# Performance work log

Hardware: AMD Instinct MI355X
Metric: run time of the kernel (lower is better)

Reference implementation:

```python
import jax, jax.numpy as jnp
import numpy as np

FEAT = 128
N_RBF = 20
CUTOFF = 5.0
N_GRAPHS = 128
ATOMS = 64
N_ATOMS = N_GRAPHS * ATOMS  # 8192
N_EDGES = N_ATOMS * 32      # 262144


def setup_inputs() -> dict:
    key = jax.random.key(0)
    ks = jax.random.split(key, 12)
    s_j = jax.random.normal(ks[0], (N_ATOMS, FEAT), jnp.float32)
    v_j = jax.random.normal(ks[1], (N_ATOMS, FEAT, 3), jnp.float32)
    r_ij = jax.random.normal(ks[2], (N_EDGES, 3), jnp.float32) * 1.5
    nbrs = jax.random.randint(ks[3], (N_EDGES, 2), 0, N_ATOMS, dtype=jnp.int32)
    num_atoms = jnp.full((N_GRAPHS,), ATOMS, dtype=jnp.int32)
    sc = 0.05
    W1 = jax.random.normal(ks[4], (FEAT, FEAT), jnp.float32) * sc
    b1 = jnp.zeros((FEAT,), jnp.float32)
    W2 = jax.random.normal(ks[5], (FEAT, 3 * FEAT), jnp.float32) * sc
    b2 = jnp.zeros((3 * FEAT,), jnp.float32)
    Wr = jax.random.normal(ks[6], (N_RBF, 3 * FEAT), jnp.float32) * sc
    br = jnp.zeros((3 * FEAT,), jnp.float32)
    Wd = jax.random.normal(ks[7], (FEAT, 3 * FEAT), jnp.float32) * sc
    bd = jnp.zeros((3 * FEAT,), jnp.float32)
    return {"s_j": s_j, "v_j": v_j, "r_ij": r_ij, "nbrs": nbrs,
            "num_atoms": num_atoms, "W1": W1, "b1": b1, "W2": W2, "b2": b2,
            "Wr": Wr, "br": br, "Wd": Wd, "bd": bd}


def _forward(s_j, v_j, r_ij, nbrs, W1, b1, W2, b2, Wr, br, Wd, bd):
    # preprocess_r
    dist = jnp.linalg.norm(r_ij, axis=-1)            # [E]
    unit = r_ij / dist[:, None]                      # [E,3]

    # InvariantMessage: per-atom MLP, gather at nbrs[:,1], times radial filter
    phi = jax.nn.silu(s_j @ W1 + b1) @ W2 + b2       # [N, 3F]
    phi_e = phi[nbrs[:, 1]]                          # [E, 3F]
    n = jnp.arange(1, N_RBF + 1, dtype=jnp.float32)
    rbf = jnp.sin(n[None, :] * jnp.pi * dist[:, None] / CUTOFF) / dist[:, None]  # [E, n_rbf]
    env = jnp.where(dist < CUTOFF, 0.5 * (jnp.cos(jnp.pi * dist / CUTOFF) + 1.0), 0.0)
    w_s = (rbf @ Wr + br) * env[:, None]             # [E, 3F]
    inv_out = (phi_e * w_s).reshape(-1, 3, FEAT)     # [E, 3, F]

    split_0 = inv_out[:, 0, :][..., None]            # [E, F, 1]
    split_1 = inv_out[:, 1, :]                       # [E, F]
    split_2 = inv_out[:, 2, :][..., None]            # [E, F, 1]

    unit_add = split_2 * unit[:, None, :]            # [E, F, 3]
    delta_v_ij = unit_add + split_0 * v_j[nbrs[:, 1]]  # [E, F, 3]
    delta_s_ij = split_1                             # [E, F]

    seg = nbrs[:, 0]
    delta_v_i = jax.ops.segment_sum(delta_v_ij, seg, num_segments=N_ATOMS)
    delta_s_l = jax.ops.segment_sum(delta_s_ij, seg, num_segments=N_ATOMS)

    # NonLocalInteraction: per-graph exact softmax attention (uniform graph size)
    qkv = s_j @ Wd + bd                              # [N, 3F]
    Q, K, V = jnp.split(qkv, 3, axis=-1)
    Qb = Q.reshape(N_GRAPHS, ATOMS, FEAT)
    Kb = K.reshape(N_GRAPHS, ATOMS, FEAT)
    Vb = V.reshape(N_GRAPHS, ATOMS, FEAT)
    scores = jnp.einsum('bqf,bkf->bqk', Qb, Kb) / jnp.sqrt(jnp.float32(FEAT))
    att = jnp.einsum('bqk,bkf->bqf', jax.nn.softmax(scores, axis=-1), Vb)
    delta_s_nl = att.reshape(N_ATOMS, FEAT)

    delta_s_i = delta_s_l + delta_s_nl
    return delta_s_i, delta_v_i


def reference(s_j, v_j, r_ij, nbrs, num_atoms, W1, b1, W2, b2, Wr, br, Wd, bd):
    # num_atoms is uniform (ATOMS per graph); attention is batched accordingly.
    return _forward(s_j, v_j, r_ij, nbrs, W1, b1, W2, b2, Wr, br, Wd, bd)
```

## Files before the change

kernel.cpp:

```cpp
#include <hip/hip_runtime.h>
#include <hip/hip_bf16.h>
#include <cstdint>

#define FEAT    128
#define NRBF    20
#define NATOMS  8192
#define NEDGES  262144
#define NGRAPH  128
#define APG     64
#define PI_F    3.14159265358979323846f
#define CUTOFF_F 5.0f
#define QTUS    ((size_t)NATOMS * 32 * 6)
#define APW     4

typedef unsigned int uint_t;
typedef unsigned short ushort_t;
typedef __attribute__((ext_vector_type(4))) float f32x4;
typedef __attribute__((ext_vector_type(4))) short short4v;
typedef __attribute__((ext_vector_type(8))) short short8;
struct U3 { uint_t x, y, z; };

__device__ __forceinline__ float bflo(uint_t u) { return __uint_as_float(u << 16); }
__device__ __forceinline__ float bfhi(uint_t u) { return __uint_as_float(u & 0xffff0000u); }
__device__ __forceinline__ float bfus(ushort_t u) { return __uint_as_float((uint_t)u << 16); }
__device__ __forceinline__ ushort_t f2bf(float f) {
  uint_t u = __float_as_uint(f);
  return (ushort_t)((u + 0x7fffu + ((u >> 16) & 1u)) >> 16);
}
__device__ __forceinline__ uint_t pack2(float lo, float hi) {
  return (uint_t)f2bf(lo) | ((uint_t)f2bf(hi) << 16);
}

__device__ __forceinline__ ushort_t swz_elem(const float* __restrict__ W, int N,
                                             int NT, int i) {
  int jj = i & 7, lane = (i >> 3) & 63, tile = i >> 9;
  int ks = tile / NT, ctg = tile - ks * NT;
  int g = lane >> 4, q = lane & 15;
  int k = 32 * ks + 4 * g + (jj & 3) + 16 * (jj >> 2);
  int c = 16 * ctg + q;
  return f2bf(W[(size_t)k * N + c]);
}

__global__ void prep_kernel(const float* __restrict__ v_j, const float* __restrict__ W1,
                            const float* __restrict__ W2, const float* __restrict__ Wd,
                            const float* __restrict__ Wr, const float* __restrict__ br,
                            const int* __restrict__ nbrs,
                            ushort_t* __restrict__ PV, ushort_t* __restrict__ w1s,
                            ushort_t* __restrict__ w2s, ushort_t* __restrict__ wds,
                            ushort_t* __restrict__ wrs, int* __restrict__ counts) {
  int i = blockIdx.x * 256 + threadIdx.x;
  if (i < NATOMS * FEAT) {
    int j = i >> 7, f = i & 127;
    int tbl = f >> 5, fl = f & 31;
    const float* vp = v_j + (size_t)i * 3;
    uint_t* o = reinterpret_cast<uint_t*>(PV + (size_t)tbl * QTUS + ((size_t)j * 32 + fl) * 6);
    o[0] = 0u;
    o[1] = pack2(0.f, vp[0]);
    o[2] = pack2(vp[1], vp[2]);
    return;
  }
  i -= NATOMS * FEAT;
  if (i < 16384) { w1s[i] = swz_elem(W1, 128, 8, i); return; }
  i -= 16384;
  if (i < 49152) { w2s[i] = swz_elem(W2, 384, 24, i); return; }
  i -= 49152;
  if (i < 49152) { wds[i] = swz_elem(Wd, 384, 24, i); return; }
  i -= 49152;
  if (i < 12288) {
    int jj = i & 7, lane = (i >> 3) & 63, ct = i >> 9;
    int g = lane >> 4, q = lane & 15;
    int k = 4 * g + (jj & 3) + 16 * (jj >> 2);
    int f = 16 * ct + q;
    float v = (k < NRBF) ? Wr[k * 384 + f] : (k == NRBF ? br[f] : 0.f);
    wrs[i] = f2bf(v);
    return;
  }
  i -= 12288;
  if (i < NEDGES) atomicAdd(&counts[nbrs[2 * i]], 1);
}

__global__ __launch_bounds__(256) void gemm_big(
    const float* __restrict__ s_j, const ushort_t* __restrict__ w1s,
    const float* __restrict__ b1, const ushort_t* __restrict__ w2s,
    const float* __restrict__ b2, const ushort_t* __restrict__ wds,
    const float* __restrict__ bd, ushort_t* __restrict__ PV,
    float* __restrict__ Qf, ushort_t* __restrict__ kvbf) {
  __shared__ ushort_t Buf[64][136];
  const int t = threadIdx.x;
  const int r0 = blockIdx.x * 64;
  const int y = blockIdx.y;
  const int w = t >> 6, l = t & 63, g = l >> 4, q = l & 15;

  for (int i = t; i < 64 * 32; i += 256) {
    int r = i >> 5, k4 = i & 31;
    float4 v = *reinterpret_cast<const float4*>(s_j + (size_t)(r0 + r) * 128 + 4 * k4);
    ushort4 o = {f2bf(v.x), f2bf(v.y), f2bf(v.z), f2bf(v.w)};
    *reinterpret_cast<ushort4*>(&Buf[r][4 * k4]) = o;
  }
  __syncthreads();

  short8 afr[4];
  #pragma unroll
  for (int ks = 0; ks < 4; ++ks) {
    const ushort_t* ap = &Buf[16 * w + q][32 * ks + 4 * g];
    short4v alo = *reinterpret_cast<const short4v*>(ap);
    short4v ahi = *reinterpret_cast<const short4v*>(ap + 16);
    afr[ks] = short8{alo[0], alo[1], alo[2], alo[3], ahi[0], ahi[1], ahi[2], ahi[3]};
  }

  if (y >= 6) {
    const int yy = y - 6;
    #pragma unroll
    for (int ct = 0; ct < 4; ++ct) {
      f32x4 acc = {};
      #pragma unroll
      for (int ks = 0; ks < 4; ++ks) {
        short8 bf = *reinterpret_cast<const short8*>(
            wds + ((size_t)(ks * 24 + yy * 4 + ct) * 64 + l) * 8);
        acc = __builtin_amdgcn_mfma_f32_16x16x32_bf16(afr[ks], bf, acc, 0, 0, 0);
      }
      int col = yy * 64 + 16 * ct + q;
      float bb = bd[col];
      #pragma unroll
      for (int r = 0; r < 4; ++r) {
        float o = acc[r] + bb;
        int row = r0 + 16 * w + 4 * g + r;
        if (col < 128) Qf[(size_t)row * 128 + col] = o;
        else           kvbf[(size_t)row * 256 + col - 128] = f2bf(o);
      }
    }
    return;
  }

  __syncthreads();
  #pragma unroll
  for (int ct = 0; ct < 8; ++ct) {
    f32x4 acc = {};
    #pragma unroll
    for (int ks = 0; ks < 4; ++ks) {
      short8 bf = *reinterpret_cast<const short8*>(
          w1s + ((size_t)(ks * 8 + ct) * 64 + l) * 8);
      acc = __builtin_amdgcn_mfma_f32_16x16x32_bf16(afr[ks], bf, acc, 0, 0, 0);
    }
    float bb = b1[16 * ct + q];
    #pragma unroll
    for (int r = 0; r < 4; ++r) {
      float o = acc[r] + bb;
      o = o / (1.f + __expf(-o));
      Buf[16 * w + 4 * g + r][16 * ct + q] = f2bf(o);
    }
  }
  __syncthreads();

  short8 hfr[4];
  #pragma unroll
  for (int ks = 0; ks < 4; ++ks) {
    const ushort_t* ap = &Buf[16 * w + q][32 * ks + 4 * g];
    short4v alo = *reinterpret_cast<const short4v*>(ap);
    short4v ahi = *reinterpret_cast<const short4v*>(ap + 16);
    hfr[ks] = short8{alo[0], alo[1], alo[2], alo[3], ahi[0], ahi[1], ahi[2], ahi[3]};
  }
  #pragma unroll
  for (int ct = 0; ct < 4; ++ct) {
    f32x4 acc = {};
    #pragma unroll
    for (int ks = 0; ks < 4; ++ks) {
      short8 bf = *reinterpret_cast<const short8*>(
          w2s + ((size_t)(ks * 24 + y * 4 + ct) * 64 + l) * 8);
      acc = __builtin_amdgcn_mfma_f32_16x16x32_bf16(hfr[ks], bf, acc, 0, 0, 0);
    }
    int col = y * 64 + 16 * ct + q;
    float bb = b2[col];
    int f = col & 127, s = col >> 7;
    int tbl = f >> 5, fl = f & 31;
    #pragma unroll
    for (int r = 0; r < 4; ++r) {
      float o = acc[r] + bb;
      int row = r0 + 16 * w + 4 * g + r;
      PV[(size_t)tbl * QTUS + ((size_t)row * 32 + fl) * 6 + s] = f2bf(o);
    }
  }
}

__global__ __launch_bounds__(1024) void scan_kernel(
    const int* __restrict__ counts, int* __restrict__ offs, int* __restrict__ cursor) {
  __shared__ int part[1024];
  const int t = threadIdx.x;
  int local[8];
  int s = 0;
  #pragma unroll
  for (int i = 0; i < 8; ++i) { local[i] = counts[t * 8 + i]; s += local[i]; }
  part[t] = s;
  __syncthreads();
  for (int off = 1; off < 1024; off <<= 1) {
    int v = part[t];
    int add = (t >= off) ? part[t - off] : 0;
    __syncthreads();
    part[t] = v + add;
    __syncthreads();
  }
  int excl = part[t] - s;
  #pragma unroll
  for (int i = 0; i < 8; ++i) {
    offs[t * 8 + i] = excl;
    cursor[t * 8 + i] = excl;
    excl += local[i];
  }
  if (t == 1023) offs[NATOMS] = excl;
}

__global__ void scatter_kernel(const int* __restrict__ nbrs, const float* __restrict__ r_ij,
                               int* __restrict__ cursor, uint4* __restrict__ erec) {
  int e = blockIdx.x * blockDim.x + threadIdx.x;
  if (e < NEDGES) {
    int2 nb = *reinterpret_cast<const int2*>(nbrs + 2 * e);
    int pos = atomicAdd(&cursor[nb.x], 1);
    const float* rp = r_ij + 3 * e;
    erec[pos] = make_uint4((uint_t)nb.y, __float_as_uint(rp[0]),
                           __float_as_uint(rp[1]), __float_as_uint(rp[2]));
  }
}

__global__ __launch_bounds__(256) void edge_mfma8(
    const uint4* __restrict__ erec, const int* __restrict__ offs,
    const ushort_t* __restrict__ PV, const ushort_t* __restrict__ wrs,
    float* __restrict__ out_s, float* __restrict__ out_v) {
  __shared__ short8 sW[6 * 64];
  const int t = threadIdx.x;
  const int qtr = blockIdx.x & 3;
  for (int i = t; i < 6 * 64; i += 256) {
    int tl = i >> 6, l2 = i & 63;
    int s = tl >> 1, c = tl & 1;
    sW[i] = *reinterpret_cast<const short8*>(
        wrs + ((size_t)(s * 8 + 2 * qtr + c) * 64 + l2) * 8);
  }
  __syncthreads();

  const int w = t >> 6, l = t & 63, g = l >> 4, q = l & 15;
  const int a0 = ((blockIdx.x >> 2) * 4 + w) * APW;
  const float c1 = PI_F / CUTOFF_F;
  const char* PVb = reinterpret_cast<const char*>(PV) + (size_t)qtr * QTUS * 2;

  int eb = offs[a0];
  int end = offs[a0 + 1];
  uint4 er = make_uint4(0u, 0u, 0u, 0u);
  if (eb + q < end) er = erec[eb + q];

  for (int aidx = 0; aidx < APW; ++aidx) {
    const int end_next = (aidx + 1 < APW) ? offs[a0 + aidx + 2] : 0;
    float ds0 = 0.f, ds1 = 0.f;
    float dv[2][3] = {};

    for (;;) {
      const bool last = (eb + 16 >= end);
      const int neb = last ? end : (eb + 16);
      const int nend = last ? ((aidx + 1 < APW) ? end_next : neb) : end;
      uint4 ern = make_uint4(0u, 0u, 0u, 0u);
      if (neb + q < nend) ern = erec[neb + q];

      float ang = 0.f, ie = 0.f, env = 0.f, u0 = 0.f, u1 = 0.f, u2 = 0.f;
      int jn = 0;
      if (eb + q < end) {
        jn = (int)er.x;
        float x = __uint_as_float(er.y), y = __uint_as_float(er.z), z = __uint_as_float(er.w);
        float d = sqrtf(x * x + y * y + z * z);
        float inv = 1.f / d;
        ang = c1 * d;
        env = (d < CUTOFF_F) ? 0.5f * (__cosf(ang) + 1.f) : 0.f;
        ie = inv * env;
        u0 = x * inv; u1 = y * inv; u2 = z * inv;
      }
      const char* pb[4];
      float ub[4][3];
      #pragma unroll
      for (int r = 0; r < 4; ++r) {
        int src = 4 * g + r;
        int jr = __shfl(jn, src, 64);
        ub[r][0] = __shfl(u0, src, 64);
        ub[r][1] = __shfl(u1, src, 64);
        ub[r][2] = __shfl(u2, src, 64);
        pb[r] = PVb + (size_t)jr * 384 + (size_t)q * 12;
      }
      U3 ld[2][4];
      #pragma unroll
      for (int c = 0; c < 2; ++c)
        #pragma unroll
        for (int r = 0; r < 4; ++r)
          ld[c][r] = *reinterpret_cast<const U3*>(pb[r] + (size_t)c * 192);
      short8 af;
      #pragma unroll
      for (int jj = 0; jj < 8; ++jj) {
        int k = 4 * g + (jj & 3) + 16 * (jj >> 2);
        float v = (k < NRBF) ? ie * __sinf((float)(k + 1) * ang)
                             : (k == NRBF ? env : 0.f);
        af[jj] = (short)f2bf(v);
      }
      #pragma unroll
      for (int c = 0; c < 2; ++c) {
        short8 b0 = sW[(0 * 2 + c) * 64 + l];
        short8 b1 = sW[(1 * 2 + c) * 64 + l];
        short8 b2 = sW[(2 * 2 + c) * 64 + l];
        f32x4 z4 = {0.f, 0.f, 0.f, 0.f};
        f32x4 cs0 = __builtin_amdgcn_mfma_f32_16x16x32_bf16(af, b0, z4, 0, 0, 0);
        f32x4 cs1 = __builtin_amdgcn_mfma_f32_16x16x32_bf16(af, b1, z4, 0, 0, 0);
        f32x4 cs2 = __builtin_amdgcn_mfma_f32_16x16x32_bf16(af, b2, z4, 0, 0, 0);
        #pragma unroll
        for (int r = 0; r < 4; ++r) {
          U3 u = ld[c][r];
          float p0 = bflo(u.x), p1 = bfhi(u.x);
          float p2 = bflo(u.y), v0 = bfhi(u.y);
          float v1 = bflo(u.z), v2 = bfhi(u.z);
          float pw0 = p0 * cs0[r];
          if (c == 0) ds0 += p1 * cs1[r]; else ds1 += p1 * cs1[r];
          float pw2 = p2 * cs2[r];
          dv[c][0] += pw0 * v0 + pw2 * ub[r][0];
          dv[c][1] += pw0 * v1 + pw2 * ub[r][1];
          dv[c][2] += pw0 * v2 + pw2 * ub[r][2];
        }
      }
      er = ern;
      eb = neb;
      if (last) break;
    }

    float r0v = ds0, r1v = ds1;
    r0v += __shfl_xor(r0v, 16, 64); r0v += __shfl_xor(r0v, 32, 64);
    r1v += __shfl_xor(r1v, 16, 64); r1v += __shfl_xor(r1v, 32, 64);
    float dvr[2][3];
    #pragma unroll
    for (int c = 0; c < 2; ++c)
      #pragma unroll
      for (int cc = 0; cc < 3; ++cc) {
        float y = dv[c][cc];
        y += __shfl_xor(y, 16, 64); y += __shfl_xor(y, 32, 64);
        dvr[c][cc] = y;
      }
    if (g < 2) {
      int atom = a0 + aidx;
      float sv = (g == 0) ? r0v : r1v;
      float d0 = (g == 0) ? dvr[0][0] : dvr[1][0];
      float d1 = (g == 0) ? dvr[0][1] : dvr[1][1];
      float d2 = (g == 0) ? dvr[0][2] : dvr[1][2];
      int f = 32 * qtr + 16 * g + q;
      out_s[(size_t)atom * FEAT + f] = sv;
      float* ov = out_v + (size_t)atom * 384 + (size_t)f * 3;
      ov[0] = d0; ov[1] = d1; ov[2] = d2;
    }
    end = end_next;
  }
}

__device__ __forceinline__ float wave_max64(float v) {
  #pragma unroll
  for (int m = 32; m > 0; m >>= 1) v = fmaxf(v, __shfl_xor(v, m, 64));
  return v;
}
__device__ __forceinline__ float wave_sum64(float v) {
  #pragma unroll
  for (int m = 32; m > 0; m >>= 1) v += __shfl_xor(v, m, 64);
  return v;
}

__global__ __launch_bounds__(256) void attn_kernel(const float* __restrict__ Qf,
                                                   const ushort_t* __restrict__ kvbf,
                                                   float* __restrict__ out_s) {
  __shared__ float4 Ks4[64 * 32];
  __shared__ float  Vs[64][130];
  __shared__ float  Ps[4][4][64];
  const int b = blockIdx.x >> 2, quad = blockIdx.x & 3;
  const int t = threadIdx.x;
  const float* qbase = Qf + (size_t)b * APG * 128;
  const ushort_t* kvb = kvbf + (size_t)b * APG * 256;

  for (int i = t; i < 64 * 32; i += 256) {
    int a = i >> 5, gg = i & 31;
    ushort4 k4 = *reinterpret_cast<const ushort4*>(kvb + a * 256 + 4 * gg);
    float4 kf = {bfus(k4.x), bfus(k4.y), bfus(k4.z), bfus(k4.w)};
    Ks4[a * 32 + (gg ^ (a & 7))] = kf;
  }
  for (int i = t; i < 64 * 32; i += 256) {
    int a = i >> 5, gg = i & 31;
    ushort4 v4 = *reinterpret_cast<const ushort4*>(kvb + a * 256 + 128 + 4 * gg);
    Vs[a][4 * gg + 0] = bfus(v4.x); Vs[a][4 * gg + 1] = bfus(v4.y);
    Vs[a][4 * gg + 2] = bfus(v4.z); Vs[a][4 * gg + 3] = bfus(v4.w);
  }
  __syncthreads();

  const int w = t >> 6, l = t & 63;
  const int qq = 4 * quad + w;
  const float scale = 0.08838834764831845f;

  const float* q0p = qbase + (size_t)(4 * qq + 0) * 128;
  const float* q1p = qbase + (size_t)(4 * qq + 1) * 128;
  const float* q2p = qbase + (size_t)(4 * qq + 2) * 128;
  const float* q3p = qbase + (size_t)(4 * qq + 3) * 128;
  float s0 = 0.f, s1 = 0.f, s2 = 0.f, s3 = 0.f;
  #pragma unroll 8
  for (int i = 0; i < 32; ++i) {
    float4 k = Ks4[l * 32 + (i ^ (l & 7))];
    float4 q0 = *reinterpret_cast<const float4*>(q0p + 4 * i);
    float4 q1 = *reinterpret_cast<const float4*>(q1p + 4 * i);
    float4 q2 = *reinterpret_cast<const float4*>(q2p + 4 * i);
    float4 q3 = *reinterpret_cast<const float4*>(q3p + 4 * i);
    s0 += q0.x * k.x + q0.y * k.y + q0.z * k.z + q0.w * k.w;
    s1 += q1.x * k.x + q1.y * k.y + q1.z * k.z + q1.w * k.w;
    s2 += q2.x * k.x + q2.y * k.y + q2.z * k.z + q2.w * k.w;
    s3 += q3.x * k.x + q3.y * k.y + q3.z * k.z + q3.w * k.w;
  }
  s0 *= scale; s1 *= scale; s2 *= scale; s3 *= scale;

  float p0 = __expf(s0 - wave_max64(s0));
  float p1 = __expf(s1 - wave_max64(s1));
  float p2 = __expf(s2 - wave_max64(s2));
  float p3 = __expf(s3 - wave_max64(s3));
  p0 /= wave_sum64(p0); p1 /= wave_sum64(p1);
  p2 /= wave_sum64(p2); p3 /= wave_sum64(p3);

  Ps[w][0][l] = p0; Ps[w][1][l] = p1; Ps[w][2][l] = p2; Ps[w][3][l] = p3;
  __threadfence_block();

  float a00 = 0.f, a01 = 0.f, a10 = 0.f, a11 = 0.f;
  float a20 = 0.f, a21 = 0.f, a30 = 0.f, a31 = 0.f;
  for (int a = 0; a < 64; ++a) {
    float2 v = *reinterpret_cast<const float2*>(&Vs[a][2 * l]);
    float pa0 = Ps[w][0][a], pa1 = Ps[w][1][a];
    float pa2 = Ps[w][2][a], pa3 = Ps[w][3][a];
    a00 += pa0 * v.x; a01 += pa0 * v.y;
    a10 += pa1 * v.x; a11 += pa1 * v.y;
    a20 += pa2 * v.x; a21 += pa2 * v.y;
    a30 += pa3 * v.x; a31 += pa3 * v.y;
  }
  size_t row0 = (size_t)(b * APG + 4 * qq) * FEAT + 2 * l;
  float2* o0 = reinterpret_cast<float2*>(out_s + row0);
  float2* o1 = reinterpret_cast<float2*>(out_s + row0 + FEAT);
  float2* o2 = reinterpret_cast<float2*>(out_s + row0 + 2 * FEAT);
  float2* o3 = reinterpret_cast<float2*>(out_s + row0 + 3 * FEAT);
  float2 c0 = *o0; c0.x += a00; c0.y += a01; *o0 = c0;
  float2 c1 = *o1; c1.x += a10; c1.y += a11; *o1 = c1;
  float2 c2 = *o2; c2.x += a20; c2.y += a21; *o2 = c2;
  float2 c3 = *o3; c3.x += a30; c3.y += a31; *o3 = c3;
}

extern "C" void kernel_launch(void* const* d_in, const int* in_sizes, int n_in,
                              void* d_out, int out_size, void* d_ws, size_t ws_size,
                              hipStream_t stream) {
  const float* s_j  = (const float*)d_in[0];
  const float* v_j  = (const float*)d_in[1];
  const float* r_ij = (const float*)d_in[2];
  const int*   nbrs = (const int*)d_in[3];
  const float* W1   = (const float*)d_in[5];
  const float* b1   = (const float*)d_in[6];
  const float* W2   = (const float*)d_in[7];
  const float* b2   = (const float*)d_in[8];
  const float* Wr   = (const float*)d_in[9];
  const float* br   = (const float*)d_in[10];
  const float* Wd   = (const float*)d_in[11];
  const float* bd   = (const float*)d_in[12];

  float* out_s = (float*)d_out;
  float* out_v = out_s + (size_t)NATOMS * FEAT;

  float*    Qf   = (float*)d_ws;
  ushort_t* kvbf = (ushort_t*)(Qf + NATOMS * FEAT);
  ushort_t* PV   = kvbf + (size_t)NATOMS * 256;
  ushort_t* w1s  = PV + 4 * QTUS;
  ushort_t* w2s  = w1s + 16384;
  ushort_t* wds  = w2s + 49152;
  ushort_t* wrs  = wds + 49152;
  uint4*    erec = (uint4*)(wrs + 12288);
  int* offs   = (int*)(erec + NEDGES);
  int* cursor = offs + (NATOMS + 1);
  int* counts = cursor + NATOMS;

  hipMemsetAsync(counts, 0, NATOMS * sizeof(int), stream);

  int prep_total = NATOMS * FEAT + 16384 + 49152 + 49152 + 12288 + NEDGES;
  prep_kernel<<<(prep_total + 255) / 256, 256, 0, stream>>>(
      v_j, W1, W2, Wd, Wr, br, nbrs, PV, w1s, w2s, wds, wrs, counts);

  scan_kernel<<<1, 1024, 0, stream>>>(counts, offs, cursor);
  scatter_kernel<<<NEDGES / 256, 256, 0, stream>>>(nbrs, r_ij, cursor, erec);

  gemm_big<<<dim3(NATOMS / 64, 12), 256, 0, stream>>>(
      s_j, w1s, b1, w2s, b2, wds, bd, PV, Qf, kvbf);

  edge_mfma8<<<NATOMS / APW, 256, 0, stream>>>(erec, offs, PV, wrs, out_s, out_v);
  attn_kernel<<<NGRAPH * 4, 256, 0, stream>>>(Qf, kvbf, out_s);
}
```

Measured before the change: 131.1 us.

## Fuse QKV projection into MLP gemm blocks and keep radial weights in registers

The gemm grid is cut from 12 to 6 y-slices, and each block now computes one 64-column slice of the QKV projection alongside its share of the W1/W2 MLP. This reuses the already staged s_j A-fragments instead of running separate blocks that reload and convert s_j. The edge kernel now loads its six radial-filter B fragments straight into registers, dropping the shared-memory staging and the __syncthreads. The trade-offs are more work per gemm block, fewer blocks in flight, and higher register pressure in the edge kernel.

```diff
diff --git a/kernel.cpp b/kernel.cpp
--- a/kernel.cpp
+++ b/kernel.cpp
@@ -107,32 +107,28 @@
     short4v ahi = *reinterpret_cast<const short4v*>(ap + 16);
     afr[ks] = short8{alo[0], alo[1], alo[2], alo[3], ahi[0], ahi[1], ahi[2], ahi[3]};
   }
-
-  if (y >= 6) {
-    const int yy = y - 6;
-    #pragma unroll
-    for (int ct = 0; ct < 4; ++ct) {
-      f32x4 acc = {};
-      #pragma unroll
-      for (int ks = 0; ks < 4; ++ks) {
-        short8 bf = *reinterpret_cast<const short8*>(
-            wds + ((size_t)(ks * 24 + yy * 4 + ct) * 64 + l) * 8);
-        acc = __builtin_amdgcn_mfma_f32_16x16x32_bf16(afr[ks], bf, acc, 0, 0, 0);
-      }
-      int col = yy * 64 + 16 * ct + q;
-      float bb = bd[col];
-      #pragma unroll
-      for (int r = 0; r < 4; ++r) {
-        float o = acc[r] + bb;
-        int row = r0 + 16 * w + 4 * g + r;
-        if (col < 128) Qf[(size_t)row * 128 + col] = o;
-        else           kvbf[(size_t)row * 256 + col - 128] = f2bf(o);
-      }
-    }
-    return;
-  }
-
   __syncthreads();
+
+  #pragma unroll
+  for (int ct = 0; ct < 4; ++ct) {
+    f32x4 acc = {};
+    #pragma unroll
+    for (int ks = 0; ks < 4; ++ks) {
+      short8 bf = *reinterpret_cast<const short8*>(
+          wds + ((size_t)(ks * 24 + y * 4 + ct) * 64 + l) * 8);
+      acc = __builtin_amdgcn_mfma_f32_16x16x32_bf16(afr[ks], bf, acc, 0, 0, 0);
+    }
+    int col = y * 64 + 16 * ct + q;
+    float bb = bd[col];
+    #pragma unroll
+    for (int r = 0; r < 4; ++r) {
+      float o = acc[r] + bb;
+      int row = r0 + 16 * w + 4 * g + r;
+      if (col < 128) Qf[(size_t)row * 128 + col] = o;
+      else           kvbf[(size_t)row * 256 + col - 128] = f2bf(o);
+    }
+  }
+
   #pragma unroll
   for (int ct = 0; ct < 8; ++ct) {
     f32x4 acc = {};
@@ -221,22 +217,22 @@
   }
 }
 
-__global__ __launch_bounds__(256) void edge_mfma8(
+__global__ __launch_bounds__(256) void edge_mfma9(
     const uint4* __restrict__ erec, const int* __restrict__ offs,
     const ushort_t* __restrict__ PV, const ushort_t* __restrict__ wrs,
     float* __restrict__ out_s, float* __restrict__ out_v) {
-  __shared__ short8 sW[6 * 64];
   const int t = threadIdx.x;
   const int qtr = blockIdx.x & 3;
-  for (int i = t; i < 6 * 64; i += 256) {
-    int tl = i >> 6, l2 = i & 63;
-    int s = tl >> 1, c = tl & 1;
-    sW[i] = *reinterpret_cast<const short8*>(
-        wrs + ((size_t)(s * 8 + 2 * qtr + c) * 64 + l2) * 8);
-  }
-  __syncthreads();
-
   const int w = t >> 6, l = t & 63, g = l >> 4, q = l & 15;
+
+  short8 Bf[3][2];
+  #pragma unroll
+  for (int s = 0; s < 3; ++s)
+    #pragma unroll
+    for (int c = 0; c < 2; ++c)
+      Bf[s][c] = *reinterpret_cast<const short8*>(
+          wrs + ((size_t)(s * 8 + 2 * qtr + c) * 64 + l) * 8);
+
   const int a0 = ((blockIdx.x >> 2) * 4 + w) * APW;
   const float c1 = PI_F / CUTOFF_F;
   const char* PVb = reinterpret_cast<const char*>(PV) + (size_t)qtr * QTUS * 2;
@@ -297,13 +293,10 @@
       }
       #pragma unroll
       for (int c = 0; c < 2; ++c) {
-        short8 b0 = sW[(0 * 2 + c) * 64 + l];
-        short8 b1 = sW[(1 * 2 + c) * 64 + l];
-        short8 b2 = sW[(2 * 2 + c) * 64 + l];
         f32x4 z4 = {0.f, 0.f, 0.f, 0.f};
-        f32x4 cs0 = __builtin_amdgcn_mfma_f32_16x16x32_bf16(af, b0, z4, 0, 0, 0);
-        f32x4 cs1 = __builtin_amdgcn_mfma_f32_16x16x32_bf16(af, b1, z4, 0, 0, 0);
-        f32x4 cs2 = __builtin_amdgcn_mfma_f32_16x16x32_bf16(af, b2, z4, 0, 0, 0);
+        f32x4 cs0 = __builtin_amdgcn_mfma_f32_16x16x32_bf16(af, Bf[0][c], z4, 0, 0, 0);
+        f32x4 cs1 = __builtin_amdgcn_mfma_f32_16x16x32_bf16(af, Bf[1][c], z4, 0, 0, 0);
+        f32x4 cs2 = __builtin_amdgcn_mfma_f32_16x16x32_bf16(af, Bf[2][c], z4, 0, 0, 0);
         #pragma unroll
         for (int r = 0; r < 4; ++r) {
           U3 u = ld[c][r];
@@ -481,9 +474,9 @@
   scan_kernel<<<1, 1024, 0, stream>>>(counts, offs, cursor);
   scatter_kernel<<<NEDGES / 256, 256, 0, stream>>>(nbrs, r_ij, cursor, erec);
 
-  gemm_big<<<dim3(NATOMS / 64, 12), 256, 0, stream>>>(
+  gemm_big<<<dim3(NATOMS / 64, 6), 256, 0, stream>>>(
       s_j, w1s, b1, w2s, b2, wds, bd, PV, Qf, kvbf);
 
-  edge_mfma8<<<NATOMS / APW, 256, 0, stream>>>(erec, offs, PV, wrs, out_s, out_v);
+  edge_mfma9<<<NATOMS / APW, 256, 0, stream>>>(erec, offs, PV, wrs, out_s, out_v);
   attn_kernel<<<NGRAPH * 4, 256, 0, stream>>>(Qf, kvbf, out_s);
 }
```

Result: no change. 129.4 us (-1.3%).
